# Performance work log

Measured on AMD Instinct MI355X. Metric: run time of the kernel, lower is better.

Reference implementation:

```python
import jax, jax.numpy as jnp
import numpy as np

N_EMBD = 256
N_HEAD = 8
HEAD_DIM = N_EMBD            # per-head dim == n_embd in this module
N_QKV = N_EMBD * N_HEAD      # 2048
B, T = 4, 2048
NEG = -1e30


def _rope(x, cos, sin):
    # x: [B, T+1, H, D]; cos/sin: [T+1, 1, D//2]
    d = x.shape[-1] // 2
    x1, x2 = x[..., :d], x[..., d:]
    y1 = x1 * cos + x2 * sin
    y2 = -x1 * sin + x2 * cos
    return jnp.concatenate([y1, y2], axis=-1)


def _rmsnorm(x):
    eps = jnp.finfo(x.dtype).eps
    return x * jax.lax.rsqrt(jnp.mean(x * x, axis=-1, keepdims=True) + eps)


def setup_inputs() -> dict:
    key = jax.random.key(0)
    k0, k1, k2, k3 = jax.random.split(key, 4)
    x = jax.random.normal(k0, (B, T, N_EMBD), jnp.float32)
    # rotary tables for T+1 positions (sink token at position 0)
    d = HEAD_DIM // 2
    pos = jnp.arange(T + 1, dtype=jnp.float32)[:, None]
    inv_freq = 1.0 / (10000.0 ** (jnp.arange(d, dtype=jnp.float32) / d))
    ang = pos * inv_freq[None, :]
    cos = jnp.cos(ang)[:, None, :]  # [T+1, 1, d]
    sin = jnp.sin(ang)[:, None, :]
    W_qkvg = jax.random.normal(k1, (4 * N_QKV, N_EMBD), jnp.float32) * 0.02
    W_sink = jax.random.normal(k2, (1, N_EMBD), jnp.float32) * 0.02
    W_out = jax.random.normal(k3, (N_EMBD, N_QKV), jnp.float32) * 0.02
    tao = jnp.array([1.2, 1.2], jnp.float32)
    return {"x": x, "cos": cos, "sin": sin, "W_qkvg": W_qkvg,
            "W_sink": W_sink, "W_out": W_out, "tao": tao, "n_head": N_HEAD}


def reference(x, cos, sin, W_qkvg, W_sink, W_out, tao, n_head):
    Bv, Tv, C = x.shape
    # prepend learned sink token
    s = jnp.broadcast_to(W_sink[None, :, :], (Bv, 1, C))
    x0 = jnp.concatenate([s, x], axis=1)                     # [B, T+1, C]
    qkvg = (x0 @ W_qkvg.T).reshape(Bv, Tv + 1, n_head, -1)   # [B, T+1, H, 4*hd]
    q, k, v, g = jnp.split(qkvg, 4, axis=-1)                 # each [B, T+1, H, hd]
    q = _rmsnorm(_rope(q, cos, sin)) * tao[0]
    k = _rmsnorm(_rope(k, cos, sin)) * tao[1]
    q, k, v, g = (a.transpose(0, 2, 1, 3) for a in (q, k, v, g))  # [B, H, T+1, hd]
    hd = q.shape[-1]
    scores = jnp.einsum("bhqd,bhkd->bhqk", q, k) / jnp.sqrt(jnp.asarray(hd, q.dtype))
    mask = jnp.tril(jnp.ones((Tv + 1, Tv + 1), bool))
    scores = jnp.where(mask, scores, NEG)
    p = jax.nn.softmax(scores, axis=-1)
    y = jnp.einsum("bhqk,bhkd->bhqd", p, v) * jax.nn.sigmoid(g)
    y = y.transpose(0, 2, 1, 3).reshape(Bv, Tv + 1, -1)[:, 1:, :]  # drop sink
    return y @ W_out.T
```

## Files before the change

### kernel.cpp

```cpp
#include <hip/hip_runtime.h>
#include <stdint.h>

#define DEVI __device__ __forceinline__

typedef __attribute__((ext_vector_type(8))) short bf16x8;
typedef __attribute__((ext_vector_type(4))) float f32x4;
typedef __attribute__((ext_vector_type(4))) unsigned short u16x4;
typedef unsigned short u16;
typedef unsigned int u32;

#define TT 2049
#define BH 32
#define MPAD 8320
#define MREAL 8196
#define NQ 8192
#define KDIM 256
#define VTP 2112

#define SBAR() __builtin_amdgcn_s_barrier()
#define MEMFENCE() asm volatile("" ::: "memory")
#define VMCNT(n) asm volatile("s_waitcnt vmcnt(" #n ")" ::: "memory")
#define LGKMCNT0() asm volatile("s_waitcnt lgkmcnt(0)" ::: "memory")

DEVI u16 f2bf(float f) {
    union { float f; u32 u; } v; v.f = f;
    u32 r = v.u + 0x7FFF + ((v.u >> 16) & 1);
    return (u16)(r >> 16);
}
DEVI float bf2f(u16 h) {
    union { u32 u; float f; } v; v.u = ((u32)h) << 16;
    return v.f;
}

#define GLD16(src, lds) __builtin_amdgcn_global_load_lds( \
    (const __attribute__((address_space(1))) void*)(src), \
    (__attribute__((address_space(3))) void*)(lds), 16, 0, 0)

#define CN0 (MPAD * 64)
#define CN1 (NQ * 64)
#define CN2 (256 * 512)
__global__ void k_conv_all(const float* __restrict__ x, const float* __restrict__ wsink,
                           const float* __restrict__ wqkvg, const float* __restrict__ wout,
                           u16* __restrict__ x0b, u16* __restrict__ wqb, u16* __restrict__ wob) {
    int idx = blockIdx.x * 256 + threadIdx.x;
    const float* src = nullptr;
    u16* dst = nullptr;
    int oidx = idx;
    bool zero_fill = false;
    if (idx < CN0) {
        int m = idx >> 6, c = (idx & 63) << 2;
        if (m < MREAL) {
            int b = m / TT, t = m - b * TT;
            src = (t == 0) ? (wsink + c) : (x + ((size_t)((b << 11) + t - 1) << 8) + c);
        } else zero_fill = true;
        dst = x0b;
    } else if (idx < CN0 + CN1) {
        oidx = idx - CN0;
        src = wqkvg + ((size_t)oidx << 2);
        dst = wqb;
    } else if (idx < CN0 + CN1 + CN2) {
        oidx = idx - CN0 - CN1;
        src = wout + ((size_t)oidx << 2);
        dst = wob;
    } else return;
    f32x4 v = {0.f, 0.f, 0.f, 0.f};
    if (!zero_fill) v = *(const f32x4*)src;
    union { u16 h[4]; uint2 u2; } o;
#pragma unroll
    for (int i = 0; i < 4; ++i) o.h[i] = f2bf(v[i]);
    *(uint2*)(dst + ((size_t)oidx << 2)) = o.u2;
}

__global__ __launch_bounds__(512) void k_gemm_qkvg(const u16* __restrict__ A, const u16* __restrict__ Bm,
                                                   const float* __restrict__ cosb, const float* __restrict__ sinb,
                                                   const float* __restrict__ tao,
                                                   u16* __restrict__ Qb, u16* __restrict__ Kb,
                                                   u16* __restrict__ Vt, u16* __restrict__ Gb) {
    __shared__ __align__(16) u16 ldsW[256 * 64];
    __shared__ __align__(16) u16 ldsX[128 * 64];
    __shared__ float rowsum[128 * 4];
    const int tid = threadIdx.x, l = tid & 63, w = tid >> 6;
    const int row0 = blockIdx.x * 128;
    const int gcol0 = blockIdx.y * 256;
    const int h = gcol0 >> 10, ty = (gcol0 & 1023) >> 8;
    const int g = w >> 1, thalf = w & 1;
    f32x4 acc[4][4];
    const f32x4 zero = {0.f, 0.f, 0.f, 0.f};
#pragma unroll
    for (int i = 0; i < 4; ++i)
#pragma unroll
        for (int j = 0; j < 4; ++j) acc[i][j] = zero;

    for (int kt = 0; kt < KDIM; kt += 64) {
        __syncthreads();
#pragma unroll
        for (int it = 0; it < 4; ++it) {
            int lin = (it * 512 + tid) * 16;
            int r = lin >> 7, cb = lin & 127;
            int scb = cb ^ ((r & 7) << 4);
            GLD16((const char*)(Bm + (size_t)(gcol0 + r) * KDIM + kt) + scb,
                  (char*)ldsW + it * 8192 + w * 1024);
        }
#pragma unroll
        for (int it = 0; it < 2; ++it) {
            int lin = (it * 512 + tid) * 16;
            int r = lin >> 7, cb = lin & 127;
            int scb = cb ^ ((r & 7) << 4);
            GLD16((const char*)(A + (size_t)(row0 + r) * KDIM + kt) + scb,
                  (char*)ldsX + it * 8192 + w * 1024);
        }
        __syncthreads();
#pragma unroll
        for (int kk = 0; kk < 64; kk += 32) {
            bf16x8 af[4], bfr[4];
            int cbyte = (kk + ((l >> 4) << 3)) * 2;
#pragma unroll
            for (int mi = 0; mi < 4; ++mi) {
                int rr = g * 32 + (mi & 1) * 16 + (mi >> 1) * 128 + (l & 15);
                af[mi] = *(const bf16x8*)((const char*)ldsW + ((rr * 128 + cbyte) ^ ((rr & 7) << 4)));
            }
#pragma unroll
            for (int ni = 0; ni < 4; ++ni) {
                int rr = thalf * 64 + ni * 16 + (l & 15);
                bfr[ni] = *(const bf16x8*)((const char*)ldsX + ((rr * 128 + cbyte) ^ ((rr & 7) << 4)));
            }
#pragma unroll
            for (int mi = 0; mi < 4; ++mi)
#pragma unroll
                for (int ni = 0; ni < 4; ++ni)
                    acc[mi][ni] = __builtin_amdgcn_mfma_f32_16x16x32_bf16(af[mi], bfr[ni], acc[mi][ni], 0, 0, 0);
        }
    }
    const float eps = 1.1920928955078125e-07f;
    if (ty < 2) {
#pragma unroll
        for (int ni = 0; ni < 4; ++ni) {
            float ss = 0.f;
#pragma unroll
            for (int mi = 0; mi < 4; ++mi)
#pragma unroll
                for (int r = 0; r < 4; ++r) { float v = acc[mi][ni][r]; ss += v * v; }
            ss += __shfl_xor(ss, 16, 64);
            ss += __shfl_xor(ss, 32, 64);
            if (l < 16) {
                int trow = thalf * 64 + ni * 16 + l;
                rowsum[trow * 4 + g] = ss;
            }
        }
        __syncthreads();
        const float tv = (ty == 0) ? tao[0] * 0.0625f : tao[1];
        u16* Obuf = (ty == 0) ? Qb : Kb;
#pragma unroll
        for (int ni = 0; ni < 4; ++ni) {
            int trow = thalf * 64 + ni * 16 + (l & 15);
            int grow = row0 + trow;
            if (grow >= MREAL) continue;
            int b = grow / TT, t = grow - b * TT;
            f32x4 rsv = *(const f32x4*)(rowsum + trow * 4);
            float rs = rsv[0] + rsv[1] + rsv[2] + rsv[3];
            float scale = rsqrtf(rs * (1.0f / 256.0f) + eps) * tv;
            u16* dst = Obuf + ((size_t)((b * 8 + h) * TT + t) << 8);
#pragma unroll
            for (int mih = 0; mih < 2; ++mih) {
                int d0 = g * 32 + mih * 16 + ((l >> 4) << 2);
                f32x4 cv = *(const f32x4*)(cosb + t * 128 + d0);
                f32x4 sv = *(const f32x4*)(sinb + t * 128 + d0);
                u16x4 lo, hi;
#pragma unroll
                for (int r = 0; r < 4; ++r) {
                    float xlo = acc[mih][ni][r], xhi = acc[mih + 2][ni][r];
                    lo[r] = f2bf((xlo * cv[r] + xhi * sv[r]) * scale);
                    hi[r] = f2bf((xhi * cv[r] - xlo * sv[r]) * scale);
                }
                *(u16x4*)(dst + d0) = lo;
                *(u16x4*)(dst + d0 + 128) = hi;
            }
        }
    } else {
#pragma unroll
        for (int ni = 0; ni < 4; ++ni) {
            int trow = thalf * 64 + ni * 16 + (l & 15);
            int grow = row0 + trow;
            if (grow >= MREAL) continue;
            int b = grow / TT, t = grow - b * TT;
            int bh = b * 8 + h;
            if (ty == 3) {
                u16* dst = Gb + ((size_t)(bh * TT + t) << 8);
#pragma unroll
                for (int mi = 0; mi < 4; ++mi) {
                    int d0 = g * 32 + (mi & 1) * 16 + (mi >> 1) * 128 + ((l >> 4) << 2);
                    u16x4 pk;
#pragma unroll
                    for (int r = 0; r < 4; ++r) pk[r] = f2bf(acc[mi][ni][r]);
                    *(u16x4*)(dst + d0) = pk;
                }
            } else {
#pragma unroll
                for (int mi = 0; mi < 4; ++mi) {
                    int d0 = g * 32 + (mi & 1) * 16 + (mi >> 1) * 128 + ((l >> 4) << 2);
#pragma unroll
                    for (int r = 0; r < 4; ++r)
                        Vt[(size_t)(bh * 256 + d0 + r) * VTP + t] = f2bf(acc[mi][ni][r]);
                }
            }
        }
    }
}

__global__ __launch_bounds__(512) void k_attn(const u16* __restrict__ Qb, const u16* __restrict__ Kb,
                                              const u16* __restrict__ Vt, const u16* __restrict__ Gb,
                                              const float* __restrict__ tao,
                                              u16* __restrict__ Y) {
    __shared__ __align__(16) u16 Kt[2][64 * 256];
    __shared__ __align__(16) u16 Vl[2][256 * 64];
    __shared__ __align__(16) u16 Plds[8][16 * 64];
    const int tid = threadIdx.x, l = tid & 63, w = tid >> 6;
    const int qt = 15 - (blockIdx.x >> 5);
    const int bh = blockIdx.x & 31;
    const int b = bh >> 3, h = bh & 7;
    const int g0 = (w >> 1) * 2;
    const int kvh = (w & 1) * 32;
    const int dh = (w & 1) * 128;
    const int mq_g0 = qt * 128 + g0 * 16 + 1;
    const size_t qkbase = (size_t)bh * TT * 256;
    const size_t vrow0 = (size_t)bh * 256;
    const float Cs = tao[0] * tao[1] * 16.0f;

    bf16x8 aq[2][8];
#pragma unroll
    for (int g = 0; g < 2; ++g) {
        int mq = mq_g0 + g * 16 + (l & 15);
        const u16* qp = Qb + qkbase + ((size_t)mq << 8) + ((l >> 4) << 3);
#pragma unroll
        for (int kk = 0; kk < 8; ++kk) aq[g][kk] = *(const bf16x8*)(qp + kk * 32);
    }
    bf16x8 vone;
#pragma unroll
    for (int i = 0; i < 8; ++i) vone[i] = (short)0x3F80;
    f32x4 acc[2][8], accs[2];
    const f32x4 zero = {0.f, 0.f, 0.f, 0.f};
#pragma unroll
    for (int g = 0; g < 2; ++g) {
#pragma unroll
        for (int i = 0; i < 8; ++i) acc[g][i] = zero;
        accs[g] = zero;
    }

    const int nkv = 2 * qt + 3;

    auto STAGE = [&](int j, int bufi) {
        const int kv0 = j << 6;
#pragma unroll
        for (int it = 0; it < 4; ++it) {
            int lin = (it * 512 + tid) * 16;
            {
                int r = lin >> 9, cbyt = lin & 511;
                int scb = cbyt ^ ((r & 7) << 4);
                int krow = kv0 + r; if (krow > 2048) krow = 2048;
                GLD16((const char*)(Kb + qkbase + ((size_t)krow << 8)) + scb,
                      (char*)&Kt[bufi][0] + it * 8192 + w * 1024);
            }
            {
                int vr = lin >> 7, cb = lin & 127;
                int scb = cb ^ ((vr & 7) << 4);
                GLD16((const char*)(Vt + (vrow0 + vr) * VTP + kv0) + scb,
                      (char*)&Vl[bufi][0] + it * 8192 + w * 1024);
            }
        }
    };

    STAGE(0, 0);
    int buf = 0;

    for (int j = 0; j < nkv; ++j) {
        const int kv0 = j << 6;
        SBAR(); MEMFENCE();
        if (j + 1 < nkv) { STAGE(j + 1, buf ^ 1); VMCNT(8); }
        else             { VMCNT(0); }
        MEMFENCE();

        const bool active = (kv0 <= mq_g0 + 31);
        if (active) {
            f32x4 s[2][2];
#pragma unroll
            for (int g = 0; g < 2; ++g) { s[g][0] = zero; s[g][1] = zero; }
            __builtin_amdgcn_s_setprio(1);
#pragma unroll
            for (int kk = 0; kk < 8; ++kk) {
                int cbyte = kk * 64 + ((l >> 4) << 4);
#pragma unroll
                for (int t = 0; t < 2; ++t) {
                    int rr = kvh + t * 16 + (l & 15);
                    bf16x8 bk = *(const bf16x8*)((const char*)&Kt[buf][0] + ((rr * 512 + cbyte) ^ ((rr & 7) << 4)));
#pragma unroll
                    for (int g = 0; g < 2; ++g)
                        s[g][t] = __builtin_amdgcn_mfma_f32_16x16x32_bf16(aq[g][kk], bk, s[g][t], 0, 0, 0);
                }
            }
            __builtin_amdgcn_s_setprio(0);
#pragma unroll
            for (int g = 0; g < 2; ++g) {
                char* pwb = (char*)&Plds[g0 + g][0];
                const bool needmask = (kv0 + kvh + 31 > mq_g0 + g * 16);
#pragma unroll
                for (int t = 0; t < 2; ++t)
#pragma unroll
                    for (int r = 0; r < 4; ++r) {
                        float sv = s[g][t][r];
                        if (needmask) {
                            int kg = kv0 + kvh + t * 16 + (l & 15);
                            int qg = mq_g0 + g * 16 + ((l >> 4) << 2) + r;
                            if (kg > qg) sv = -1e30f;
                        }
                        float pv = __expf(sv - Cs);
                        int row = ((l >> 4) << 2) + r;
                        int byte = row * 128 + (kvh + t * 16 + (l & 15)) * 2;
                        *(u16*)(pwb + (byte ^ ((row & 7) << 4))) = f2bf(pv);
                    }
            }
        }
        LGKMCNT0(); SBAR(); MEMFENCE();

        if (active) {
            bf16x8 ap[2][2];
#pragma unroll
            for (int g = 0; g < 2; ++g) {
                const char* prb = (const char*)&Plds[g0 + g][0];
                int row = l & 15;
                int b0 = row * 128 + ((l >> 4) << 4);
                ap[g][0] = *(const bf16x8*)(prb + (b0 ^ ((row & 7) << 4)));
                ap[g][1] = *(const bf16x8*)(prb + ((b0 + 64) ^ ((row & 7) << 4)));
            }
            __builtin_amdgcn_s_setprio(1);
#pragma unroll
            for (int df = 0; df < 8; ++df) {
                int vr = dh + df * 16 + (l & 15);
                int cbase = vr * 128 + ((l >> 4) << 4);
                bf16x8 bv0 = *(const bf16x8*)((const char*)&Vl[buf][0] + (cbase ^ ((vr & 7) << 4)));
                bf16x8 bv1 = *(const bf16x8*)((const char*)&Vl[buf][0] + ((cbase + 64) ^ ((vr & 7) << 4)));
#pragma unroll
                for (int g = 0; g < 2; ++g) {
                    acc[g][df] = __builtin_amdgcn_mfma_f32_16x16x32_bf16(ap[g][0], bv0, acc[g][df], 0, 0, 0);
                    acc[g][df] = __builtin_amdgcn_mfma_f32_16x16x32_bf16(ap[g][1], bv1, acc[g][df], 0, 0, 0);
                }
            }
#pragma unroll
            for (int g = 0; g < 2; ++g) {
                accs[g] = __builtin_amdgcn_mfma_f32_16x16x32_bf16(ap[g][0], vone, accs[g], 0, 0, 0);
                accs[g] = __builtin_amdgcn_mfma_f32_16x16x32_bf16(ap[g][1], vone, accs[g], 0, 0, 0);
            }
            __builtin_amdgcn_s_setprio(0);
        }
        buf ^= 1;
    }
#pragma unroll
    for (int g = 0; g < 2; ++g)
#pragma unroll
        for (int r = 0; r < 4; ++r) {
            int mq = mq_g0 + g * 16 + ((l >> 4) << 2) + r;
            float inv = 1.0f / accs[g][r];
            const u16* gp = Gb + qkbase + ((size_t)mq << 8) + dh + (l & 15);
            u16* yp = Y + ((size_t)(b * 2048 + mq - 1)) * 2048 + h * 256 + dh + (l & 15);
#pragma unroll
            for (int df = 0; df < 8; ++df) {
                float g2 = bf2f(gp[df * 16]);
                float sg = 1.0f / (1.0f + __expf(-g2));
                yp[df * 16] = f2bf(acc[g][df][r] * inv * sg);
            }
        }
}

__global__ __launch_bounds__(256) void k_gemm_out(const u16* __restrict__ A, const u16* __restrict__ Bm,
                                                  float* __restrict__ Cout) {
    __shared__ __align__(16) u16 ldsA[64 * 64];
    __shared__ __align__(16) u16 ldsB[64 * 64];
    const int tid = threadIdx.x;
    const int l = tid & 63, w = tid >> 6;
    const int row0 = blockIdx.x * 64, col0 = blockIdx.y * 64;
    const int mbase = (w >> 1) * 32, nbase = (w & 1) * 32;
    const int K2 = 2048;
    f32x4 acc[2][2];
    const f32x4 zero = {0.f, 0.f, 0.f, 0.f};
#pragma unroll
    for (int i = 0; i < 2; ++i)
#pragma unroll
        for (int j = 0; j < 2; ++j) acc[i][j] = zero;

    for (int kt = 0; kt < K2; kt += 64) {
        __syncthreads();
#pragma unroll
        for (int it = 0; it < 2; ++it) {
            int lin = (it * 256 + tid) * 16;
            int r = lin >> 7;
            int cb = lin & 127;
            int scb = cb ^ ((r & 7) << 4);
            GLD16((const char*)(A + (size_t)(row0 + r) * K2 + kt) + scb,
                  (char*)ldsA + it * 4096 + w * 1024);
            GLD16((const char*)(Bm + (size_t)(col0 + r) * K2 + kt) + scb,
                  (char*)ldsB + it * 4096 + w * 1024);
        }
        __syncthreads();
#pragma unroll
        for (int kk = 0; kk < 64; kk += 32) {
            bf16x8 af[2], bfr[2];
            int cbyte = (kk + ((l >> 4) << 3)) * 2;
#pragma unroll
            for (int mi = 0; mi < 2; ++mi) {
                int rr = mbase + mi * 16 + (l & 15);
                af[mi] = *(const bf16x8*)((const char*)ldsA + ((rr * 128 + cbyte) ^ ((rr & 7) << 4)));
            }
#pragma unroll
            for (int ni = 0; ni < 2; ++ni) {
                int rr = nbase + ni * 16 + (l & 15);
                bfr[ni] = *(const bf16x8*)((const char*)ldsB + ((rr * 128 + cbyte) ^ ((rr & 7) << 4)));
            }
#pragma unroll
            for (int mi = 0; mi < 2; ++mi)
#pragma unroll
                for (int ni = 0; ni < 2; ++ni)
                    acc[mi][ni] = __builtin_amdgcn_mfma_f32_16x16x32_bf16(af[mi], bfr[ni], acc[mi][ni], 0, 0, 0);
        }
    }
#pragma unroll
    for (int mi = 0; mi < 2; ++mi)
#pragma unroll
        for (int ni = 0; ni < 2; ++ni)
#pragma unroll
            for (int r = 0; r < 4; ++r) {
                int grow = row0 + mbase + mi * 16 + ((l >> 4) << 2) + r;
                int gcol = col0 + nbase + ni * 16 + (l & 15);
                Cout[(size_t)grow * 256 + gcol] = acc[mi][ni][r];
            }
}

extern "C" void kernel_launch(void* const* d_in, const int* in_sizes, int n_in,
                              void* d_out, int out_size, void* d_ws, size_t ws_size,
                              hipStream_t stream) {
    const float* x     = (const float*)d_in[0];
    const float* cosb  = (const float*)d_in[1];
    const float* sinb  = (const float*)d_in[2];
    const float* wqkvg = (const float*)d_in[3];
    const float* wsink = (const float*)d_in[4];
    const float* wout  = (const float*)d_in[5];
    const float* tao   = (const float*)d_in[6];
    float* out = (float*)d_out;

    char* ws = (char*)d_ws;
    u16* x0b = (u16*)(ws + 0);
    u16* wqb = (u16*)(ws + 4259840);
    u16* wob = (u16*)(ws + 8454144);
    u16* Qb  = (u16*)(ws + 9502720);
    u16* Kb  = (u16*)(ws + 43073536);
    u16* Gb  = (u16*)(ws + 76644352);
    u16* Vt  = (u16*)(ws + 110215168);
    u16* Yb  = (u16*)(ws + 144818176);

    k_conv_all<<<dim3((CN0 + CN1 + CN2 + 255) / 256), 256, 0, stream>>>(
        x, wsink, wqkvg, wout, x0b, wqb, wob);
    k_gemm_qkvg<<<dim3(65, 32), 512, 0, stream>>>(x0b, wqb, cosb, sinb, tao, Qb, Kb, Vt, Gb);
    k_attn<<<dim3(16 * 32), 512, 0, stream>>>(Qb, Kb, Vt, Gb, tao, Yb);
    k_gemm_out<<<dim3(128, 4), 256, 0, stream>>>(Yb, wob, out);
}
```

Measured before the change: 227.7 us.

## Stage V transpose through LDS for coalesced stores and use exp2 softmax

The V output of the projection kernel is now transposed through shared memory with an XOR swizzle, so each wavefront writes contiguous runs along t of the Vt layout. Previously every element was a scattered 2-byte global store with a large stride. Separately, log2(e) is folded into the Q scale and the softmax constant so the attention kernel can call exp2f instead of __expf. The LDS staging adds extra barriers and reuses the weight LDS buffer.

```diff
diff --git a/kernel.cpp b/kernel.cpp
--- a/kernel.cpp
+++ b/kernel.cpp
@@ -148,7 +148,7 @@
             }
         }
         __syncthreads();
-        const float tv = (ty == 0) ? tao[0] * 0.0625f : tao[1];
+        const float tv = (ty == 0) ? tao[0] * 0.0625f * 1.44269504f : tao[1];
         u16* Obuf = (ty == 0) ? Qb : Kb;
 #pragma unroll
         for (int ni = 0; ni < 4; ++ni) {
@@ -176,7 +176,7 @@
                 *(u16x4*)(dst + d0 + 128) = hi;
             }
         }
-    } else {
+    } else if (ty == 3) {
 #pragma unroll
         for (int ni = 0; ni < 4; ++ni) {
             int trow = thalf * 64 + ni * 16 + (l & 15);
@@ -184,25 +184,52 @@
             if (grow >= MREAL) continue;
             int b = grow / TT, t = grow - b * TT;
             int bh = b * 8 + h;
-            if (ty == 3) {
-                u16* dst = Gb + ((size_t)(bh * TT + t) << 8);
-#pragma unroll
-                for (int mi = 0; mi < 4; ++mi) {
-                    int d0 = g * 32 + (mi & 1) * 16 + (mi >> 1) * 128 + ((l >> 4) << 2);
-                    u16x4 pk;
-#pragma unroll
-                    for (int r = 0; r < 4; ++r) pk[r] = f2bf(acc[mi][ni][r]);
-                    *(u16x4*)(dst + d0) = pk;
+            u16* dst = Gb + ((size_t)(bh * TT + t) << 8);
+#pragma unroll
+            for (int mi = 0; mi < 4; ++mi) {
+                int d0 = g * 32 + (mi & 1) * 16 + (mi >> 1) * 128 + ((l >> 4) << 2);
+                u16x4 pk;
+#pragma unroll
+                for (int r = 0; r < 4; ++r) pk[r] = f2bf(acc[mi][ni][r]);
+                *(u16x4*)(dst + d0) = pk;
+            }
+        }
+    } else {
+        char* Ct = (char*)ldsW;
+        __syncthreads();
+        int grow0 = row0 + l, grow1 = row0 + l + 64;
+        int b0_ = grow0 / TT, t0_ = grow0 - b0_ * TT;
+        int b1_ = grow1 / TT, t1_ = grow1 - b1_ * TT;
+        bool v0 = grow0 < MREAL, v1 = grow1 < MREAL;
+#pragma unroll
+        for (int half = 0; half < 2; ++half) {
+#pragma unroll
+            for (int mi2 = 0; mi2 < 2; ++mi2) {
+                int mi = half * 2 + mi2;
+#pragma unroll
+                for (int ni = 0; ni < 4; ++ni) {
+                    int t = thalf * 64 + ni * 16 + (l & 15);
+#pragma unroll
+                    for (int r = 0; r < 4; ++r) {
+                        int dd = g * 32 + (mi & 1) * 16 + ((l >> 4) << 2) + r;
+                        int byte = (dd * 256 + t * 2) ^ (((dd >> 2) & 7) << 4);
+                        *(u16*)(Ct + byte) = f2bf(acc[mi][ni][r]);
+                    }
                 }
-            } else {
-#pragma unroll
-                for (int mi = 0; mi < 4; ++mi) {
-                    int d0 = g * 32 + (mi & 1) * 16 + (mi >> 1) * 128 + ((l >> 4) << 2);
-#pragma unroll
-                    for (int r = 0; r < 4; ++r)
-                        Vt[(size_t)(bh * 256 + d0 + r) * VTP + t] = f2bf(acc[mi][ni][r]);
-                }
-            }
+            }
+            __syncthreads();
+#pragma unroll
+            for (int p = 0; p < 16; ++p) {
+                int dloc = p * 8 + w;
+                int d = half * 128 + dloc;
+                int byte0 = (dloc * 256 + l * 2) ^ (((dloc >> 2) & 7) << 4);
+                int byte1 = (dloc * 256 + (l + 64) * 2) ^ (((dloc >> 2) & 7) << 4);
+                u16 q0 = *(const u16*)(Ct + byte0);
+                u16 q1 = *(const u16*)(Ct + byte1);
+                if (v0) Vt[((size_t)((b0_ * 8 + h) * 256 + d)) * VTP + t0_] = q0;
+                if (v1) Vt[((size_t)((b1_ * 8 + h) * 256 + d)) * VTP + t1_] = q1;
+            }
+            if (half == 0) __syncthreads();
         }
     }
 }
@@ -224,7 +251,7 @@
     const int mq_g0 = qt * 128 + g0 * 16 + 1;
     const size_t qkbase = (size_t)bh * TT * 256;
     const size_t vrow0 = (size_t)bh * 256;
-    const float Cs = tao[0] * tao[1] * 16.0f;
+    const float Cs2 = tao[0] * tao[1] * 16.0f * 1.44269504f;
 
     bf16x8 aq[2][8];
 #pragma unroll
@@ -312,7 +339,7 @@
                             int qg = mq_g0 + g * 16 + ((l >> 4) << 2) + r;
                             if (kg > qg) sv = -1e30f;
                         }
-                        float pv = __expf(sv - Cs);
+                        float pv = exp2f(sv - Cs2);
                         int row = ((l >> 4) << 2) + r;
                         int byte = row * 128 + (kvh + t * 16 + (l & 15)) * 2;
                         *(u16*)(pwb + (byte ^ ((row & 7) << 4))) = f2bf(pv);
```

After: 245.4 us. +7.8%, slower.
